# Optimization experiments

Measured on AMD Instinct MI355X. Metric: run time of the kernel, lower is better.

Reference implementation:

```python
import jax, jax.numpy as jnp
import numpy as np

B, H, W = 2, 512, 512
HID, NHKD, HEADS, KD, CD = 64, 128, 8, 16, 64
MAX_SHAPE = 512

def _conv(x, w, b=None, pad=0, groups=1):
    y = jax.lax.conv_general_dilated(x, w, (1, 1), [(pad, pad), (pad, pad)],
                                     dimension_numbers=('NCHW', 'OIHW', 'NCHW'),
                                     feature_group_count=groups)
    return y if b is None else y + b[None, :, None, None]

def _gelu(x):
    return jax.nn.gelu(x, approximate=False)  # torch nn.GELU default is exact erf

def _bn(x, s, t):
    # inference-mode BatchNorm folded to per-channel scale/shift
    return x * s[None, :, None, None] + t[None, :, None, None]

def _dyn_pos(xm, pe):
    # xm: (B, C, N); pe: (1, C, MAX_SHAPE); linear interp (align_corners=False) when N != MAX_SHAPE
    N = xm.shape[-1]
    if N != pe.shape[-1]:
        pe = jax.image.resize(pe, (1, pe.shape[1], N), method='linear')
    return xm + pe

def _sdpa(q, k, v):
    # q, k, v: (B, heads, L=key_dim, E=H); scale = 1/sqrt(E) as in F.scaled_dot_product_attention
    scale = 1.0 / np.sqrt(q.shape[-1])
    attn = jax.nn.softmax(jnp.einsum('bhie,bhje->bhij', q, k) * scale, axis=-1)
    return jnp.einsum('bhij,bhje->bhie', attn, v)

def setup_inputs():
    key = jax.random.key(0)
    ks = jax.random.split(key, 26)
    rn = lambda i, shp, sc=1.0: jax.random.normal(ks[i], shp, jnp.float32) * sc
    return {
        'x': rn(0, (B, HID, H, W)),
        'shortcut': rn(1, (B, CD, H, W)),
        'ln_w': jnp.ones((CD,), jnp.float32),
        'ln_b': jnp.zeros((CD,), jnp.float32),
        'dproj_dw_w': rn(2, (CD, 1, 3, 3), 0.2),
        'dproj_bn_s': 1.0 + rn(3, (CD,), 0.1),
        'dproj_bn_t': rn(4, (CD,), 0.1),
        'dproj_pw_w': rn(5, (2 * HID, CD, 1, 1), 0.125),
        'dproj_pw_b': rn(6, (2 * HID,), 0.05),
        'q_dw_w': rn(7, (NHKD, 1, 3, 3), 0.2),
        'q_bn_s': 1.0 + rn(8, (NHKD,), 0.1),
        'q_bn_t': rn(9, (NHKD,), 0.1),
        'k_dw_w': rn(10, (NHKD, 1, 3, 3), 0.2),
        'k_bn_s': 1.0 + rn(11, (NHKD,), 0.1),
        'k_bn_t': rn(12, (NHKD,), 0.1),
        'v_pw_w': rn(13, (NHKD, HID, 1, 1), 0.125),
        'v_bn_s': 1.0 + rn(14, (NHKD,), 0.1),
        'v_bn_t': rn(15, (NHKD,), 0.1),
        'proj_dw_w': rn(16, (HID + 2 * NHKD, 1, 3, 3), 0.2),
        'proj_dw_b': rn(17, (HID + 2 * NHKD,), 0.05),
        'proj_pw_w': rn(18, (HID, HID + 2 * NHKD, 1, 1), 0.06),
        'proj_pw_b': rn(19, (HID,), 0.05),
        'pe_rowq': rn(20, (1, NHKD, MAX_SHAPE), 0.02),
        'pe_rowk': rn(21, (1, NHKD, MAX_SHAPE), 0.02),
        'pe_colq': rn(22, (1, NHKD, MAX_SHAPE), 0.02),
        'pe_colk': rn(23, (1, NHKD, MAX_SHAPE), 0.02),
        'ape_row_w': jnp.ones((1, NHKD, 1, 1), jnp.float32),
        'ape_col_w': jnp.ones((1, NHKD, 1, 1), jnp.float32),
    }

def reference(x, shortcut, ln_w, ln_b, dproj_dw_w, dproj_bn_s, dproj_bn_t,
              dproj_pw_w, dproj_pw_b, q_dw_w, q_bn_s, q_bn_t, k_dw_w, k_bn_s,
              k_bn_t, v_pw_w, v_bn_s, v_bn_t, proj_dw_w, proj_dw_b, proj_pw_w,
              proj_pw_b, pe_rowq, pe_rowk, pe_colq, pe_colk, ape_row_w, ape_col_w):
    b, _, h, w = x.shape
    # LayerNorm2d: normalize over channel axis (biased variance, eps=1e-5)
    mu = shortcut.mean(axis=1, keepdims=True)
    var = shortcut.var(axis=1, keepdims=True)
    sn = (shortcut - mu) / jnp.sqrt(var + 1e-5) * ln_w[None, :, None, None] + ln_b[None, :, None, None]
    # d_proj: dw3x3 -> BN -> GELU -> pw1x1 -> GELU
    s = _gelu(_bn(_conv(sn, dproj_dw_w, pad=1, groups=CD), dproj_bn_s, dproj_bn_t))
    s = _gelu(_conv(s, dproj_pw_w, dproj_pw_b))
    k_in, v_in = jnp.split(s, 2, axis=1)  # each (B, HID, H, W)
    # q/k: grouped 3x3 conv (groups=HID, out=NHKD) -> BN -> GELU; v: 1x1 -> BN
    q = _gelu(_bn(_conv(x, q_dw_w, pad=1, groups=HID), q_bn_s, q_bn_t))
    k = _gelu(_bn(_conv(k_in, k_dw_w, pad=1, groups=HID), k_bn_s, k_bn_t))
    v = _bn(_conv(v_in, v_pw_w), v_bn_s, v_bn_t)
    # row attention: pool over W, seq dim = key_dim (16), head dim = H
    qr = _dyn_pos(q.mean(-1), pe_rowq).reshape(b, HEADS, KD, h)
    kr = _dyn_pos(k.mean(-1), pe_rowk).reshape(b, HEADS, KD, h)
    vr = v.mean(-1).reshape(b, HEADS, KD, h)
    attn_row = _sdpa(qr, kr, vr).reshape(b, NHKD, 1, h)
    # column attention: pool over H
    qc = _dyn_pos(q.mean(-2), pe_colq).reshape(b, HEADS, KD, w)
    kc = _dyn_pos(k.mean(-2), pe_colk).reshape(b, HEADS, KD, w)
    vc = v.mean(-2).reshape(b, HEADS, KD, w)
    attn_col = _sdpa(qc, kc, vc).reshape(b, NHKD, 1, w)
    # AxialPositionEncoding: both maps broadcast over spatial axis 2 (requires H == W)
    attn = v + ape_row_w * attn_row + ape_col_w * attn_col
    cat = jnp.concatenate([x, attn, v], axis=1)  # (B, 320, H, W)
    ctot = cat.shape[1]
    # channel shuffle: 'b (c g) h w -> b (g c) h w', g=5
    shuf = cat.reshape(b, ctot // 5, 5, h, w).transpose(0, 2, 1, 3, 4).reshape(b, ctot, h, w)
    p = _gelu(_conv(shuf, proj_dw_w, proj_dw_b, pad=1, groups=ctot))
    p = _conv(p, proj_pw_w, proj_pw_b)
    return _gelu(p)
```

## Files before the change

### kernel.cpp

```cpp
#include <hip/hip_runtime.h>
#include <math.h>

#define PLANE (512*512)

typedef short bf16x8 __attribute__((ext_vector_type(8)));
typedef float f32x4 __attribute__((ext_vector_type(4)));

__device__ __forceinline__ float gelu_f(float x) {
    float ax = fabsf(x) * 0.70710678118654752440f;
    float t = __builtin_amdgcn_rcpf(1.0f + 0.3275911f * ax);
    float poly = t * (0.254829592f + t * (-0.284496736f + t * (1.421413741f
               + t * (-1.453152027f + t * 1.061405429f))));
    float e = __expf(-ax * ax);
    float er = 1.0f - poly * e;
    er = copysignf(er, x);
    return 0.5f * x * (1.0f + er);
}

__device__ __forceinline__ unsigned short f2bf(float f) {
    union { float f; unsigned u; } v; v.f = f;
    unsigned r = v.u + 0x7FFFu + ((v.u >> 16) & 1u);
    return (unsigned short)(r >> 16);
}

__device__ __forceinline__ float bf2f(unsigned short u) {
    union { unsigned u; float f; } x; x.u = ((unsigned)u) << 16; return x.f;
}

__device__ __forceinline__ float ldval(const float* p, int off) { return p[off]; }
__device__ __forceinline__ float ldval(const unsigned short* p, int off) { return bf2f(p[off]); }

__global__ __launch_bounds__(256) void k_lnstats(const float* __restrict__ sc,
                                                 float* __restrict__ Pb,
                                                 float* __restrict__ Qb) {
    int p = blockIdx.x * 256 + threadIdx.x;
    int b = p >> 18;
    int hw = p & (PLANE - 1);
    const float* src = sc + (size_t)b * 64 * PLANE + hw;
    float sum = 0.f, sq = 0.f;
    #pragma unroll 8
    for (int c = 0; c < 64; ++c) {
        float v = src[(size_t)c * PLANE];
        sum += v; sq += v * v;
    }
    float mu = sum * (1.0f / 64.0f);
    float var = sq * (1.0f / 64.0f) - mu * mu;
    float rstd = rsqrtf(var + 1e-5f);
    Pb[p] = rstd;
    Qb[p] = -mu * rstd;
}

__global__ __launch_bounds__(256) void k_dw64ln(const float* __restrict__ sc,
                                                const float* __restrict__ dww,
                                                const float* __restrict__ lnw,
                                                const float* __restrict__ lnb,
                                                const float* __restrict__ bns,
                                                const float* __restrict__ bnt,
                                                const float* __restrict__ Pb,
                                                const float* __restrict__ Qb,
                                                unsigned* __restrict__ t1b) {
    int p = blockIdx.x * 256 + threadIdx.x;
    int b = p >> 18;
    int hw = p & (PLANE - 1);
    int h = hw >> 9, w = hw & 511;
    int tapoff[9]; float Pt[9], Qt[9], vm[9];
    const float* Pp = Pb + (size_t)b * PLANE;
    const float* Qp = Qb + (size_t)b * PLANE;
    #pragma unroll
    for (int dh = -1; dh <= 1; ++dh)
        #pragma unroll
        for (int dw = -1; dw <= 1; ++dw) {
            int k = (dh + 1) * 3 + dw + 1;
            int hh = h + dh, ww = w + dw;
            bool ok = (hh >= 0 && hh < 512 && ww >= 0 && ww < 511 + 1);
            ok = (hh >= 0 && hh < 512 && ww >= 0 && ww < 512);
            int hc = ok ? hh : h, wc = ok ? ww : w;
            int off = hc * 512 + wc;
            tapoff[k] = off;
            vm[k] = ok ? 1.f : 0.f;
            Pt[k] = Pp[off]; Qt[k] = Qp[off];
        }
    const float* scb = sc + (size_t)b * 64 * PLANE;
    unsigned* ob = t1b + (size_t)b * 32 * PLANE + hw;
    for (int c2 = 0; c2 < 32; ++c2) {
        float g[2];
        #pragma unroll
        for (int e = 0; e < 2; ++e) {
            int c = c2 * 2 + e;
            const float* wp = dww + c * 9;
            const float* cp = scb + (size_t)c * PLANE;
            float conv = 0.f, wsum = 0.f;
            #pragma unroll
            for (int k = 0; k < 9; ++k) {
                float wv = wp[k];
                float raw = cp[tapoff[k]];
                conv = fmaf(wv, fmaf(raw, Pt[k], Qt[k]) * vm[k], conv);
                wsum = fmaf(wv, vm[k], wsum);
            }
            float a = lnw[c] * conv + lnb[c] * wsum;
            g[e] = gelu_f(a * bns[c] + bnt[c]);
        }
        unsigned r;
        asm("v_cvt_pk_bf16_f32 %0,%1,%2" : "=v"(r) : "v"(g[0]), "v"(g[1]));
        ob[(size_t)c2 * PLANE] = r;
    }
}

__global__ __launch_bounds__(256) void k_wsetup2(const float* __restrict__ W1,
                                                 const float* __restrict__ W2,
                                                 unsigned short* __restrict__ w1b,
                                                 unsigned short* __restrict__ w2b) {
    int tid = blockIdx.x * 256 + threadIdx.x;
    if (tid < 8192) { w1b[tid] = f2bf(W1[tid]); w2b[tid] = f2bf(W2[tid]); }
}

__global__ __launch_bounds__(256, 4) void k_pw2(
    const unsigned* __restrict__ t1b,
    const unsigned short* __restrict__ w1b, const float* __restrict__ b1,
    const unsigned short* __restrict__ w2b,
    const float* __restrict__ vbs, const float* __restrict__ vbt,
    unsigned short* __restrict__ k_in, unsigned short* __restrict__ v)
{
    __shared__ unsigned short vin[64][88];
    __shared__ float epi[64 * 68];
    __shared__ float psl[128], ptl[128], pbl[128];
    int tid = threadIdx.x;
    if (tid < 128) { psl[tid] = vbs[tid]; ptl[tid] = vbt[tid]; pbl[tid] = b1[tid]; }
    int lane = tid & 63, wva = tid >> 6;
    int cl = lane & 15, kg = lane >> 4;
    int p0 = blockIdx.x * 64;
    int b = p0 >> 18;
    int hw0 = p0 & (PLANE - 1);
    int px = wva * 16 + cl;
    const unsigned* tp = t1b + (size_t)b * 32 * PLANE + hw0 + px;
    __syncthreads();

    unsigned bfr[2][4];
    #pragma unroll
    for (int ks = 0; ks < 2; ++ks)
        #pragma unroll
        for (int jp = 0; jp < 4; ++jp)
            bfr[ks][jp] = tp[(size_t)(ks * 16 + kg * 4 + jp) * PLANE];

    f32x4 acc[8];
    #pragma unroll
    for (int mt = 0; mt < 8; ++mt) acc[mt] = (f32x4){0.f, 0.f, 0.f, 0.f};
    #pragma unroll
    for (int ks = 0; ks < 2; ++ks) {
        union { unsigned u[4]; bf16x8 v; } bb;
        bb.u[0] = bfr[ks][0]; bb.u[1] = bfr[ks][1]; bb.u[2] = bfr[ks][2]; bb.u[3] = bfr[ks][3];
        #pragma unroll
        for (int mt = 0; mt < 8; ++mt) {
            bf16x8 af = *(const bf16x8*)(w1b + (size_t)(mt * 16 + cl) * 64 + ks * 32 + kg * 8);
            acc[mt] = __builtin_amdgcn_mfma_f32_16x16x32_bf16(af, bb.v, acc[mt], 0, 0, 0);
        }
    }

    #pragma unroll
    for (int mt = 4; mt < 8; ++mt) {
        float g[4];
        #pragma unroll
        for (int r = 0; r < 4; ++r)
            g[r] = gelu_f(acc[mt][r] + pbl[mt * 16 + kg * 4 + r]);
        unsigned r01, r23;
        asm("v_cvt_pk_bf16_f32 %0,%1,%2" : "=v"(r01) : "v"(g[0]), "v"(g[1]));
        asm("v_cvt_pk_bf16_f32 %0,%1,%2" : "=v"(r23) : "v"(g[2]), "v"(g[3]));
        int ch = (mt - 4) * 16 + kg * 4;
        *(unsigned*)&vin[px][ch]     = r01;
        *(unsigned*)&vin[px][ch + 2] = r23;
    }

    __syncthreads();
    #pragma unroll
    for (int mt = 0; mt < 4; ++mt)
        #pragma unroll
        for (int r = 0; r < 4; ++r) {
            int m = mt * 16 + kg * 4 + r;
            epi[m * 68 + px] = gelu_f(acc[mt][r] + pbl[m]);
        }
    __syncthreads();
    unsigned short* kb = k_in + (size_t)b * 64 * PLANE + hw0;
    #pragma unroll
    for (int k = 0; k < 4; ++k) {
        int m = wva * 16 + k * 4 + kg;
        float4 vv = *(const float4*)&epi[m * 68 + cl * 4];
        unsigned r01, r23;
        asm("v_cvt_pk_bf16_f32 %0,%1,%2" : "=v"(r01) : "v"(vv.x), "v"(vv.y));
        asm("v_cvt_pk_bf16_f32 %0,%1,%2" : "=v"(r23) : "v"(vv.z), "v"(vv.w));
        uint2 st; st.x = r01; st.y = r23;
        *(uint2*)&kb[(size_t)m * PLANE + cl * 4] = st;
    }

    f32x4 acc2[8];
    #pragma unroll
    for (int mt = 0; mt < 8; ++mt) acc2[mt] = (f32x4){0.f, 0.f, 0.f, 0.f};
    #pragma unroll
    for (int ks = 0; ks < 2; ++ks) {
        bf16x8 bb = *(const bf16x8*)&vin[px][ks * 32 + kg * 8];
        #pragma unroll
        for (int mt = 0; mt < 8; ++mt) {
            bf16x8 af = *(const bf16x8*)(w2b + (size_t)(mt * 16 + cl) * 64 + ks * 32 + kg * 8);
            acc2[mt] = __builtin_amdgcn_mfma_f32_16x16x32_bf16(af, bb, acc2[mt], 0, 0, 0);
        }
    }

    unsigned short* vb = v + (size_t)b * 128 * PLANE + hw0;
    #pragma unroll
    for (int pass = 0; pass < 2; ++pass) {
        __syncthreads();
        #pragma unroll
        for (int mt = pass * 4; mt < pass * 4 + 4; ++mt)
            #pragma unroll
            for (int r = 0; r < 4; ++r) {
                int m = mt * 16 + kg * 4 + r;
                epi[(m - pass * 64) * 68 + px] = acc2[mt][r] * psl[m] + ptl[m];
            }
        __syncthreads();
        #pragma unroll
        for (int k = 0; k < 4; ++k) {
            int ml = wva * 16 + k * 4 + kg;
            float4 vv = *(const float4*)&epi[ml * 68 + cl * 4];
            unsigned r01, r23;
            asm("v_cvt_pk_bf16_f32 %0,%1,%2" : "=v"(r01) : "v"(vv.x), "v"(vv.y));
            asm("v_cvt_pk_bf16_f32 %0,%1,%2" : "=v"(r23) : "v"(vv.z), "v"(vv.w));
            uint2 st; st.x = r01; st.y = r23;
            *(uint2*)&vb[(size_t)(pass * 64 + ml) * PLANE + cl * 4] = st;
        }
    }
}

template<typename T>
__global__ __launch_bounds__(512) void k_dwpool(const T* __restrict__ in,
                                                const float* __restrict__ wt,
                                                const float* __restrict__ bns,
                                                const float* __restrict__ bnt,
                                                float* __restrict__ rowsum,
                                                float* __restrict__ colpart) {
    __shared__ float lred[2][64][8];
    int tid = threadIdx.x;
    int blk = blockIdx.x;
    int hc = blk & 7;
    int g  = (blk >> 3) & 63;
    int b  = blk >> 9;
    int o0 = 2 * g, o1 = o0 + 1;
    const T* ip = in + ((size_t)b * 64 + g) * PLANE;
    float w0[9], w1[9];
    #pragma unroll
    for (int k = 0; k < 9; ++k) { w0[k] = wt[o0 * 9 + k]; w1[k] = wt[o1 * 9 + k]; }
    float s0 = bns[o0], t0 = bnt[o0], s1 = bns[o1], tt1 = bnt[o1];
    int w = tid;
    int wm = (w > 0)   ? w - 1 : w;  float vm0 = (w > 0)   ? 1.f : 0.f;
    int wp = (w < 511) ? w + 1 : w;  float vm2 = (w < 511) ? 1.f : 0.f;
    int h0 = hc * 64;
    int lane = tid & 63, wv = tid >> 6;
    float a0, a1, a2, r0, r1, r2, c0, c1, c2;
    if (h0 >= 1) {
        int o = (h0 - 1) * 512;
        a0 = ldval(ip, o + wm) * vm0; a1 = ldval(ip, o + w); a2 = ldval(ip, o + wp) * vm2;
    } else { a0 = a1 = a2 = 0.f; }
    {
        int o = h0 * 512;
        r0 = ldval(ip, o + wm) * vm0; r1 = ldval(ip, o + w); r2 = ldval(ip, o + wp) * vm2;
    }
    float ca0 = 0.f, ca1 = 0.f;
    for (int r = 0; r < 64; ++r) {
        int h = h0 + r;
        if (h + 1 <= 511) {
            int o = (h + 1) * 512;
            c0 = ldval(ip, o + wm) * vm0; c1 = ldval(ip, o + w); c2 = ldval(ip, o + wp) * vm2;
        } else { c0 = c1 = c2 = 0.f; }
        float x0 = w0[0]*a0 + w0[1]*a1 + w0[2]*a2 + w0[3]*r0 + w0[4]*r1 + w0[5]*r2
                 + w0[6]*c0 + w0[7]*c1 + w0[8]*c2;
        float x1 = w1[0]*a0 + w1[1]*a1 + w1[2]*a2 + w1[3]*r0 + w1[4]*r1 + w1[5]*r2
                 + w1[6]*c0 + w1[7]*c1 + w1[8]*c2;
        x0 = gelu_f(x0 * s0 + t0);
        x1 = gelu_f(x1 * s1 + tt1);
        ca0 += x0; ca1 += x1;
        #pragma unroll
        for (int off = 32; off > 0; off >>= 1) {
            x0 += __shfl_down(x0, off, 64);
            x1 += __shfl_down(x1, off, 64);
        }
        if (lane == 0) { lred[0][r][wv] = x0; lred[1][r][wv] = x1; }
        a0 = r0; a1 = r1; a2 = r2; r0 = c0; r1 = c1; r2 = c2;
    }
    colpart[((size_t)(b * 128 + o0) * 8 + hc) * 512 + w] = ca0;
    colpart[((size_t)(b * 128 + o1) * 8 + hc) * 512 + w] = ca1;
    __syncthreads();
    if (tid < 128) {
        int oo = tid >> 6, r = tid & 63;
        float s = 0.f;
        #pragma unroll
        for (int i = 0; i < 8; ++i) s += lred[oo][r][i];
        int och = oo ? o1 : o0;
        rowsum[((size_t)b * 128 + och) * 512 + h0 + r] = s;
    }
}

__global__ __launch_bounds__(512) void k_vpool(const unsigned short* __restrict__ v,
                                               float* __restrict__ rowsum,
                                               float* __restrict__ colpart) {
    __shared__ float lred[64][8];
    int tid = threadIdx.x;
    int blk = blockIdx.x;
    int hc = blk & 7;
    int c  = (blk >> 3) & 127;
    int b  = blk >> 10;
    int bc = b * 128 + c;
    const unsigned short* ip = v + (size_t)bc * PLANE;
    int h0 = hc * 64;
    int lane = tid & 63, wv = tid >> 6;
    float ca = 0.f;
    for (int r = 0; r < 64; ++r) {
        float a = bf2f(ip[(h0 + r) * 512 + tid]);
        ca += a;
        #pragma unroll
        for (int off = 32; off > 0; off >>= 1) a += __shfl_down(a, off, 64);
        if (lane == 0) lred[r][wv] = a;
    }
    colpart[((size_t)bc * 8 + hc) * 512 + tid] = ca;
    __syncthreads();
    if (tid < 64) {
        float s = 0.f;
        #pragma unroll
        for (int i = 0; i < 8; ++i) s += lred[tid][i];
        rowsum[(size_t)bc * 512 + h0 + tid] = s;
    }
}

__global__ __launch_bounds__(256) void k_colreduce(const float* __restrict__ part,
                                                   float* __restrict__ out, int n) {
    int idx = blockIdx.x * 256 + threadIdx.x;
    if (idx >= n) return;
    int bc = idx >> 9, w = idx & 511;
    const float* pp = part + ((size_t)bc * 8) * 512 + w;
    float s = 0.f;
    #pragma unroll
    for (int p = 0; p < 8; ++p) s += pp[p * 512];
    out[idx] = s;
}

__global__ __launch_bounds__(256) void k_attn(const float* __restrict__ qrow,
                                              const float* __restrict__ krow,
                                              const float* __restrict__ vrow,
                                              const float* __restrict__ qcol,
                                              const float* __restrict__ kcol,
                                              const float* __restrict__ vcol,
                                              const float* __restrict__ perq,
                                              const float* __restrict__ perk,
                                              const float* __restrict__ pecq,
                                              const float* __restrict__ peck,
                                              float* __restrict__ arow,
                                              float* __restrict__ acol) {
    __shared__ float P[16][17];
    int blk = blockIdx.x;
    int axis = blk & 1;
    int head = (blk >> 1) & 7;
    int b = blk >> 4;
    const float* qs = axis ? qcol : qrow;
    const float* ks = axis ? kcol : krow;
    const float* vs = axis ? vcol : vrow;
    const float* peq = axis ? pecq : perq;
    const float* pek = axis ? peck : perk;
    float* out = axis ? acol : arow;
    int tid = threadIdx.x;
    int i = tid >> 4, j = tid & 15;
    int ci = head * 16 + i, cj = head * 16 + j;
    const float* qp = qs + ((size_t)b * 128 + ci) * 512;
    const float* kp = ks + ((size_t)b * 128 + cj) * 512;
    const float* qe = peq + ci * 512;
    const float* ke = pek + cj * 512;
    float s = 0.f;
    for (int n = 0; n < 512; ++n) {
        float qv = qp[n] * (1.f / 512.f) + qe[n];
        float kv = kp[n] * (1.f / 512.f) + ke[n];
        s += qv * kv;
    }
    s *= 0.0441941738241592203f;
    P[i][j] = s;
    __syncthreads();
    if (tid < 16) {
        float mx = -1e30f;
        #pragma unroll
        for (int jj = 0; jj < 16; ++jj) mx = fmaxf(mx, P[tid][jj]);
        float e[16];
        float sum = 0.f;
        #pragma unroll
        for (int jj = 0; jj < 16; ++jj) { e[jj] = expf(P[tid][jj] - mx); sum += e[jj]; }
        float inv = 1.f / sum;
        #pragma unroll
        for (int jj = 0; jj < 16; ++jj) P[tid][jj] = e[jj] * inv;
    }
    __syncthreads();
    for (int idx = tid; idx < 16 * 512; idx += 256) {
        int ii = idx >> 9, n = idx & 511;
        const float* vb = vs + ((size_t)b * 128 + head * 16) * 512 + n;
        float acc = 0.f;
        #pragma unroll
        for (int jj = 0; jj < 16; ++jj) acc += P[ii][jj] * vb[jj * 512] * (1.f / 512.f);
        out[((size_t)b * 128 + head * 16 + ii) * 512 + n] = acc;
    }
}

__global__ __launch_bounds__(256) void k_wsetup(const float* __restrict__ pww,
                                                unsigned short* __restrict__ wsh) {
    int tid = blockIdx.x * 256 + threadIdx.x;
    if (tid >= 64 * 320) return;
    int m = tid / 320, src = tid % 320;
    int o = (src % 5) * 64 + src / 5;
    wsh[m * 320 + src] = f2bf(pww[m * 320 + o]);
}

__global__ __launch_bounds__(256) void k_awsetup(const float* __restrict__ pdw,
                                                 const float* __restrict__ aprw,
                                                 const float* __restrict__ apcw,
                                                 const float* __restrict__ arow,
                                                 const float* __restrict__ acol,
                                                 float* __restrict__ aw) {
    int idx = blockIdx.x * 256 + threadIdx.x;
    if (idx >= 2 * 128 * 512) return;
    int col = idx & 511;
    int c   = (idx >> 9) & 127;
    int b   = idx >> 16;
    int src = 64 + c;
    int o = (src % 5) * 64 + src / 5;
    const float* wd = pdw + o * 9;
    float ws0 = wd[0] + wd[3] + wd[6];
    float ws1 = wd[1] + wd[4] + wd[7];
    float ws2 = wd[2] + wd[5] + wd[8];
    const float* ar = arow + ((size_t)b * 128 + c) * 512;
    const float* ac = acol + ((size_t)b * 128 + c) * 512;
    float apr = aprw[c], apc = apcw[c];
    float sum = ws1 * (apr * ar[col] + apc * ac[col]);
    if (col > 0)   sum += ws0 * (apr * ar[col - 1] + apc * ac[col - 1]);
    if (col < 511) sum += ws2 * (apr * ar[col + 1] + apc * ac[col + 1]);
    aw[idx] = sum;
}

template<bool HE, bool WE>
__device__ __forceinline__ void conv2x2b(const unsigned short* __restrict__ p,
    const float* wlA, const float* wlP,
    const int* hrow, const float* rv, int ls, int rs, float cv0, float cv2,
    float outA[2], float outP[2])
{
    float a0,a1,a2, b0,b1,b2, c0,c1,c2;
    const unsigned short* q = p + hrow[0]*512;
    if (WE) { a0=bf2f(q[ls])*cv0; a1=bf2f(q[0]); a2=bf2f(q[rs])*cv2; } else { a0=bf2f(q[-1]); a1=bf2f(q[0]); a2=bf2f(q[1]); }
    q = p + hrow[1]*512;
    if (WE) { b0=bf2f(q[ls])*cv0; b1=bf2f(q[0]); b2=bf2f(q[rs])*cv2; } else { b0=bf2f(q[-1]); b1=bf2f(q[0]); b2=bf2f(q[1]); }
    q = p + hrow[2]*512;
    if (WE) { c0=bf2f(q[ls])*cv0; c1=bf2f(q[0]); c2=bf2f(q[rs])*cv2; } else { c0=bf2f(q[-1]); c1=bf2f(q[0]); c2=bf2f(q[1]); }
    #pragma unroll
    for (int hs = 0; hs < 2; ++hs) {
        float sA0 = wlA[0]*a0 + wlA[1]*a1 + wlA[2]*a2;
        float sA1 = wlA[3]*b0 + wlA[4]*b1 + wlA[5]*b2;
        float sA2 = wlA[6]*c0 + wlA[7]*c1 + wlA[8]*c2;
        float sP0 = wlP[0]*a0 + wlP[1]*a1 + wlP[2]*a2;
        float sP1 = wlP[3]*b0 + wlP[4]*b1 + wlP[5]*b2;
        float sP2 = wlP[6]*c0 + wlP[7]*c1 + wlP[8]*c2;
        if (HE) {
            outA[hs] = rv[hs]*sA0 + sA1 + rv[hs+2]*sA2 + wlA[9];
            outP[hs] = rv[hs]*sP0 + sP1 + rv[hs+2]*sP2 + wlP[9];
        } else {
            outA[hs] = sA0 + sA1 + sA2 + wlA[9];
            outP[hs] = sP0 + sP1 + sP2 + wlP[9];
        }
        if (hs < 1) {
            a0=b0; a1=b1; a2=b2; b0=c0; b1=c1; b2=c2;
            q = p + hrow[3]*512;
            if (WE) { c0=bf2f(q[ls])*cv0; c1=bf2f(q[0]); c2=bf2f(q[rs])*cv2; } else { c0=bf2f(q[-1]); c1=bf2f(q[0]); c2=bf2f(q[1]); }
        }
    }
}

template<bool HE, bool WE>
__device__ __forceinline__ void conv1x2(const float* __restrict__ p,
    const float* wl,
    const int* hrow, const float* rv, int ls, int rs, float cv0, float cv2,
    float out[2])
{
    float a0,a1,a2, b0,b1,b2, c0,c1,c2;
    const float* q = p + hrow[0]*512;
    if (WE) { a0=q[ls]*cv0; a1=q[0]; a2=q[rs]*cv2; } else { a0=q[-1]; a1=q[0]; a2=q[1]; }
    q = p + hrow[1]*512;
    if (WE) { b0=q[ls]*cv0; b1=q[0]; b2=q[rs]*cv2; } else { b0=q[-1]; b1=q[0]; b2=q[1]; }
    q = p + hrow[2]*512;
    if (WE) { c0=q[ls]*cv0; c1=q[0]; c2=q[rs]*cv2; } else { c0=q[-1]; c1=q[0]; c2=q[1]; }
    #pragma unroll
    for (int hs = 0; hs < 2; ++hs) {
        float s0 = wl[0]*a0 + wl[1]*a1 + wl[2]*a2;
        float s1 = wl[3]*b0 + wl[4]*b1 + wl[5]*b2;
        float s2 = wl[6]*c0 + wl[7]*c1 + wl[8]*c2;
        out[hs] = (HE ? (rv[hs]*s0 + s1 + rv[hs+2]*s2) : (s0 + s1 + s2)) + wl[9];
        if (hs < 1) {
            a0=b0; a1=b1; a2=b2; b0=c0; b1=c1; b2=c2;
            q = p + hrow[3]*512;
            if (WE) { c0=q[ls]*cv0; c1=q[0]; c2=q[rs]*cv2; } else { c0=q[-1]; c1=q[0]; c2=q[1]; }
        }
    }
}

template<bool HE, bool WE>
__device__ __forceinline__ void proj5_core(
    int h0, int wwbase, float* epi, const float* dwl,
    const float* __restrict__ xb, const unsigned short* __restrict__ vbp,
    const float* __restrict__ arb, const float* __restrict__ acb,
    const float* __restrict__ aprw, const float* __restrict__ apcw,
    const float* __restrict__ awb,
    const unsigned short* __restrict__ wsh, const float* __restrict__ pwb,
    float* __restrict__ outb)
{
    int tid = threadIdx.x;
    int lane = tid & 63, wva = tid >> 6;
    int cl = lane & 15, kg = lane >> 4;
    int ww = wwbase + wva * 16 + cl;

    int hrow[4]; float rv[4];
    #pragma unroll
    for (int i = 0; i < 4; ++i) {
        int r = h0 - 1 + i;
        float va = 1.f;
        if (HE) { if (r < 0) { r = 0; va = 0.f; } if (r > 511) { r = 511; va = 0.f; } }
        hrow[i] = r; rv[i] = va;
    }
    int ls = -1, rs = 1; float cv0 = 1.f, cv2 = 1.f;
    if (WE) {
        if (ww == 0)   { ls = 1;  cv0 = 0.f; }
        if (ww == 511) { rs = -1; cv2 = 0.f; }
    }

    f32x4 acc[2][4];
    #pragma unroll
    for (int hs = 0; hs < 2; ++hs)
        #pragma unroll
        for (int mt = 0; mt < 4; ++mt)
            acc[hs][mt] = (f32x4){0.f, 0.f, 0.f, 0.f};

    #pragma unroll
    for (int ks = 0; ks < 2; ++ks) {
        unsigned bp[2][4];
        #pragma unroll
        for (int jp = 0; jp < 4; ++jp) {
            float cj0[2], cj1[2];
            int ch = ks * 32 + kg * 8 + jp * 2;
            conv1x2<HE,WE>(xb + (size_t)ch * PLANE + ww, dwl + ch * 12,
                           hrow, rv, ls, rs, cv0, cv2, cj0);
            conv1x2<HE,WE>(xb + (size_t)(ch+1) * PLANE + ww, dwl + (ch+1) * 12,
                           hrow, rv, ls, rs, cv0, cv2, cj1);
            #pragma unroll
            for (int hs = 0; hs < 2; ++hs) {
                float g0 = gelu_f(cj0[hs]), g1 = gelu_f(cj1[hs]);
                unsigned r;
                asm("v_cvt_pk_bf16_f32 %0,%1,%2" : "=v"(r) : "v"(g0), "v"(g1));
                bp[hs][jp] = r;
            }
        }
        #pragma unroll
        for (int mt = 0; mt < 4; ++mt) {
            bf16x8 af = *(const bf16x8*)(wsh + (size_t)(mt * 16 + cl) * 320 + ks * 32 + kg * 8);
            #pragma unroll
            for (int hs = 0; hs < 2; ++hs) {
                union { unsigned u[4]; bf16x8 v; } bb;
                bb.u[0] = bp[hs][0]; bb.u[1] = bp[hs][1]; bb.u[2] = bp[hs][2]; bb.u[3] = bp[hs][3];
                acc[hs][mt] = __builtin_amdgcn_mfma_f32_16x16x32_bf16(af, bb.v, acc[hs][mt], 0, 0, 0);
            }
        }
    }

    #pragma unroll
    for (int vks = 0; vks < 4; ++vks) {
        unsigned bpA[2][4], bpP[2][4];
        #pragma unroll
        for (int jp = 0; jp < 4; ++jp) {
            float cA[2][2], cP[2][2];
            #pragma unroll
            for (int e = 0; e < 2; ++e) {
                int c = vks * 32 + kg * 8 + jp * 2 + e;
                const float* wlA = dwl + (64 + c) * 12;
                conv2x2b<HE,WE>(vbp + (size_t)c * PLANE + ww, wlA, dwl + (192 + c) * 12,
                                hrow, rv, ls, rs, cv0, cv2, cA[e], cP[e]);
                float awv = awb[(size_t)c * 512 + ww];
                #pragma unroll
                for (int hs = 0; hs < 2; ++hs) {
                    if (!HE) {
                        cA[e][hs] += awv;
                    } else {
                        if (rv[hs] + rv[hs + 2] == 2.f) {
                            cA[e][hs] += awv;
                        } else {
                            const float* arp = arb + (size_t)c * 512 + ww;
                            const float* acp = acb + (size_t)c * 512 + ww;
                            float apr = aprw[c], apc = apcw[c];
                            float aa0 = (apr * arp[ls] + apc * acp[ls]) * cv0;
                            float aa1 =  apr * arp[0]  + apc * acp[0];
                            float aa2 = (apr * arp[rs] + apc * acp[rs]) * cv2;
                            float wd0 = rv[hs]*wlA[0] + wlA[3] + rv[hs+2]*wlA[6];
                            float wd1 = rv[hs]*wlA[1] + wlA[4] + rv[hs+2]*wlA[7];
                            float wd2 = rv[hs]*wlA[2] + wlA[5] + rv[hs+2]*wlA[8];
                            cA[e][hs] += wd0*aa0 + wd1*aa1 + wd2*aa2;
                        }
                    }
                }
            }
            #pragma unroll
            for (int hs = 0; hs < 2; ++hs) {
                float gA0 = gelu_f(cA[0][hs]), gA1 = gelu_f(cA[1][hs]);
                float gP0 = gelu_f(cP[0][hs]), gP1 = gelu_f(cP[1][hs]);
                unsigned ra, rp;
                asm("v_cvt_pk_bf16_f32 %0,%1,%2" : "=v"(ra) : "v"(gA0), "v"(gA1));
                asm("v_cvt_pk_bf16_f32 %0,%1,%2" : "=v"(rp) : "v"(gP0), "v"(gP1));
                bpA[hs][jp] = ra; bpP[hs][jp] = rp;
            }
        }
        #pragma unroll
        for (int mt = 0; mt < 4; ++mt) {
            bf16x8 afA = *(const bf16x8*)(wsh + (size_t)(mt * 16 + cl) * 320 + (2 + vks) * 32 + kg * 8);
            #pragma unroll
            for (int hs = 0; hs < 2; ++hs) {
                union { unsigned u[4]; bf16x8 v; } bb;
                bb.u[0] = bpA[hs][0]; bb.u[1] = bpA[hs][1]; bb.u[2] = bpA[hs][2]; bb.u[3] = bpA[hs][3];
                acc[hs][mt] = __builtin_amdgcn_mfma_f32_16x16x32_bf16(afA, bb.v, acc[hs][mt], 0, 0, 0);
            }
            bf16x8 afP = *(const bf16x8*)(wsh + (size_t)(mt * 16 + cl) * 320 + (6 + vks) * 32 + kg * 8);
            #pragma unroll
            for (int hs = 0; hs < 2; ++hs) {
                union { unsigned u[4]; bf16x8 v; } bb;
                bb.u[0] = bpP[hs][0]; bb.u[1] = bpP[hs][1]; bb.u[2] = bpP[hs][2]; bb.u[3] = bpP[hs][3];
                acc[hs][mt] = __builtin_amdgcn_mfma_f32_16x16x32_bf16(afP, bb.v, acc[hs][mt], 0, 0, 0);
            }
        }
    }

    #pragma unroll
    for (int hs = 0; hs < 2; ++hs) {
        __syncthreads();
        #pragma unroll
        for (int mt = 0; mt < 4; ++mt)
            #pragma unroll
            for (int r = 0; r < 4; ++r) {
                int m = mt * 16 + kg * 4 + r;
                epi[m * 68 + wva * 16 + cl] = gelu_f(acc[hs][mt][r] + pwb[m]);
            }
        __syncthreads();
        #pragma unroll
        for (int k = 0; k < 4; ++k) {
            int m = wva * 16 + k * 4 + kg;
            float4 vv = *(const float4*)&epi[m * 68 + cl * 4];
            *(float4*)&outb[(size_t)m * PLANE + (size_t)(h0 + hs) * 512 + wwbase + cl * 4] = vv;
        }
    }
}

__global__ __launch_bounds__(256, 4) void k_proj5(
    const float* __restrict__ x, const unsigned short* __restrict__ v,
    const float* __restrict__ arow, const float* __restrict__ acol,
    const float* __restrict__ aprw, const float* __restrict__ apcw,
    const float* __restrict__ dww, const float* __restrict__ dwb,
    const unsigned short* __restrict__ wsh, const float* __restrict__ pwb,
    const float* __restrict__ aw, float* __restrict__ out)
{
    __shared__ float dwl[320 * 12];
    __shared__ float epi[64 * 68];
    int tid = threadIdx.x;
    for (int i = tid; i < 3200; i += 256) {
        int src = i / 10, k = i - src * 10;
        int o = (src % 5) * 64 + src / 5;
        dwl[src * 12 + k] = (k < 9) ? dww[o * 9 + k] : dwb[o];
    }
    __syncthreads();
    int flat = blockIdx.x;
    int nf = (flat & 7) * 512 + (flat >> 3);
    int bx = nf & 7;
    int s  = (nf >> 3) & 255;
    int b  = nf >> 11;
    int h0 = s * 2, wwbase = bx * 64;
    const float* xb  = x + (size_t)b * 64 * PLANE;
    const unsigned short* vbp = v + (size_t)b * 128 * PLANE;
    const float* arb = arow + (size_t)b * 128 * 512;
    const float* acb = acol + (size_t)b * 128 * 512;
    const float* awb = aw + (size_t)b * 128 * 512;
    float* outb = out + (size_t)b * 64 * PLANE;
    bool HEr = (s == 0) || (s == 255);
    bool WEr = (bx == 0) || (bx == 7);
    if (!HEr && !WEr)
        proj5_core<false,false>(h0, wwbase, epi, dwl, xb, vbp, arb, acb, aprw, apcw, awb, wsh, pwb, outb);
    else if (!HEr)
        proj5_core<false,true >(h0, wwbase, epi, dwl, xb, vbp, arb, acb, aprw, apcw, awb, wsh, pwb, outb);
    else
        proj5_core<true ,true >(h0, wwbase, epi, dwl, xb, vbp, arb, acb, aprw, apcw, awb, wsh, pwb, outb);
}

extern "C" void kernel_launch(void* const* d_in, const int* in_sizes, int n_in,
                              void* d_out, int out_size, void* d_ws, size_t ws_size,
                              hipStream_t stream) {
    const float* x    = (const float*)d_in[0];
    const float* sc   = (const float*)d_in[1];
    const float* lnw  = (const float*)d_in[2];
    const float* lnb  = (const float*)d_in[3];
    const float* ddw  = (const float*)d_in[4];
    const float* dbs  = (const float*)d_in[5];
    const float* dbt  = (const float*)d_in[6];
    const float* pw1  = (const float*)d_in[7];
    const float* pb1  = (const float*)d_in[8];
    const float* qdw  = (const float*)d_in[9];
    const float* qbs  = (const float*)d_in[10];
    const float* qbt  = (const float*)d_in[11];
    const float* kdw  = (const float*)d_in[12];
    const float* kbs  = (const float*)d_in[13];
    const float* kbt  = (const float*)d_in[14];
    const float* vpw  = (const float*)d_in[15];
    const float* vbs  = (const float*)d_in[16];
    const float* vbt  = (const float*)d_in[17];
    const float* pdw  = (const float*)d_in[18];
    const float* pdb  = (const float*)d_in[19];
    const float* ppw  = (const float*)d_in[20];
    const float* ppb  = (const float*)d_in[21];
    const float* perq = (const float*)d_in[22];
    const float* perk = (const float*)d_in[23];
    const float* pecq = (const float*)d_in[24];
    const float* peck = (const float*)d_in[25];
    const float* aprw = (const float*)d_in[26];
    const float* apcw = (const float*)d_in[27];

    unsigned short* kin_b = (unsigned short*)d_out;
    float* ws   = (float*)d_ws;
    float* bufB = ws;
    unsigned short* v_b = (unsigned short*)(ws + 33554432);
    float* sm   = ws + 100663296;
    float* qrow = sm;
    float* krow = sm + 131072;
    float* vrow = sm + 262144;
    float* qcol = sm + 393216;
    float* kcol = sm + 524288;
    float* vcol = sm + 655360;
    float* arow = sm + 786432;
    float* acol = sm + 917504;
    unsigned short* wsh = (unsigned short*)(ws + 101711872);
    float* aw   = ws + 101722112;
    unsigned short* w1b = (unsigned short*)(ws + 101853184);
    unsigned short* w2b = (unsigned short*)(ws + 101857280);
    float* Pb   = ws + 101861376;
    float* Qb   = ws + 102385664;
    unsigned* t1b = (unsigned*)bufB;
    float* qcp  = bufB;
    float* kcp  = bufB + 1048576;
    float* vcp  = bufB + 2097152;

    k_wsetup <<<80,   256, 0, stream>>>(ppw, wsh);
    k_wsetup2<<<32,   256, 0, stream>>>(pw1, vpw, w1b, w2b);
    k_lnstats<<<2048, 256, 0, stream>>>(sc, Pb, Qb);
    k_dw64ln <<<2048, 256, 0, stream>>>(sc, ddw, lnw, lnb, dbs, dbt, Pb, Qb, t1b);
    k_pw2    <<<8192, 256, 0, stream>>>(t1b, w1b, pb1, w2b, vbs, vbt, kin_b, v_b);
    k_dwpool<unsigned short><<<1024, 512, 0, stream>>>(kin_b, kdw, kbs, kbt, krow, kcp);
    k_vpool  <<<2048, 512, 0, stream>>>(v_b, vrow, vcp);
    k_dwpool<float><<<1024, 512, 0, stream>>>(x, qdw, qbs, qbt, qrow, qcp);
    k_colreduce<<<1536, 256, 0, stream>>>(qcp, qcol, 393216);
    k_attn   <<<32,   256, 0, stream>>>(qrow, krow, vrow, qcol, kcol, vcol,
                                        perq, perk, pecq, peck, arow, acol);
    k_awsetup<<<512,  256, 0, stream>>>(pdw, aprw, apcw, arow, acol, aw);
    k_proj5  <<<4096, 256, 0, stream>>>(x, v_b, arow, acol, aprw, apcw,
                                        pdw, pdb, wsh, ppb, aw, (float*)d_out);
}
```

Measured before the change: 912.6 us.

## Parallelize axial attention across query rows and use tanh-form GELU

The attention kernel now launches one block per (batch, axis, head, query row) and splits each QK dot product across 16 lanes with a shuffle reduction, replacing 32 blocks of long serial loops. Softmax normalization is folded into the output scaling. GELU switches from the erf polynomial to a cheaper sigmoid-based tanh approximation, which changes numerics relative to exact erf GELU. The new attention recomputes the per-head V pass redundantly per query row.

```diff
diff --git a/kernel.cpp b/kernel.cpp
--- a/kernel.cpp
+++ b/kernel.cpp
@@ -7,14 +7,10 @@
 typedef float f32x4 __attribute__((ext_vector_type(4)));
 
 __device__ __forceinline__ float gelu_f(float x) {
-    float ax = fabsf(x) * 0.70710678118654752440f;
-    float t = __builtin_amdgcn_rcpf(1.0f + 0.3275911f * ax);
-    float poly = t * (0.254829592f + t * (-0.284496736f + t * (1.421413741f
-               + t * (-1.453152027f + t * 1.061405429f))));
-    float e = __expf(-ax * ax);
-    float er = 1.0f - poly * e;
-    er = copysignf(er, x);
-    return 0.5f * x * (1.0f + er);
+    float t2 = fmaf(x * x, 0.0713548162f, 1.5957691216f);
+    float e = __expf(x * t2);
+    float r = __builtin_amdgcn_rcpf(1.0f + e);
+    return fmaf(-x, r, x);
 }
 
 __device__ __forceinline__ unsigned short f2bf(float f) {
@@ -72,8 +68,7 @@
         for (int dw = -1; dw <= 1; ++dw) {
             int k = (dh + 1) * 3 + dw + 1;
             int hh = h + dh, ww = w + dw;
-            bool ok = (hh >= 0 && hh < 512 && ww >= 0 && ww < 511 + 1);
-            ok = (hh >= 0 && hh < 512 && ww >= 0 && ww < 512);
+            bool ok = (hh >= 0 && hh < 512 && ww >= 0 && ww < 512);
             int hc = ok ? hh : h, wc = ok ? ww : w;
             int off = hc * 512 + wc;
             tapoff[k] = off;
@@ -352,11 +347,13 @@
                                               const float* __restrict__ peck,
                                               float* __restrict__ arow,
                                               float* __restrict__ acol) {
-    __shared__ float P[16][17];
+    __shared__ float Pj[16];
+    __shared__ float Pe[16];
     int blk = blockIdx.x;
-    int axis = blk & 1;
-    int head = (blk >> 1) & 7;
-    int b = blk >> 4;
+    int i    = blk & 15;
+    int head = (blk >> 4) & 7;
+    int axis = (blk >> 7) & 1;
+    int b    = blk >> 8;
     const float* qs = axis ? qcol : qrow;
     const float* ks = axis ? kcol : krow;
     const float* vs = axis ? vcol : vrow;
@@ -364,41 +361,44 @@
     const float* pek = axis ? peck : perk;
     float* out = axis ? acol : arow;
     int tid = threadIdx.x;
-    int i = tid >> 4, j = tid & 15;
+    int j = tid >> 4, l = tid & 15;
     int ci = head * 16 + i, cj = head * 16 + j;
     const float* qp = qs + ((size_t)b * 128 + ci) * 512;
     const float* kp = ks + ((size_t)b * 128 + cj) * 512;
     const float* qe = peq + ci * 512;
     const float* ke = pek + cj * 512;
     float s = 0.f;
-    for (int n = 0; n < 512; ++n) {
+    int n0 = l * 32;
+    for (int n = n0; n < n0 + 32; ++n) {
         float qv = qp[n] * (1.f / 512.f) + qe[n];
         float kv = kp[n] * (1.f / 512.f) + ke[n];
-        s += qv * kv;
-    }
-    s *= 0.0441941738241592203f;
-    P[i][j] = s;
+        s = fmaf(qv, kv, s);
+    }
+    #pragma unroll
+    for (int off = 8; off > 0; off >>= 1) s += __shfl_down(s, off, 16);
+    if (l == 0) Pj[j] = s * 0.0441941738241592203f;
     __syncthreads();
     if (tid < 16) {
         float mx = -1e30f;
         #pragma unroll
-        for (int jj = 0; jj < 16; ++jj) mx = fmaxf(mx, P[tid][jj]);
-        float e[16];
-        float sum = 0.f;
-        #pragma unroll
-        for (int jj = 0; jj < 16; ++jj) { e[jj] = expf(P[tid][jj] - mx); sum += e[jj]; }
-        float inv = 1.f / sum;
-        #pragma unroll
-        for (int jj = 0; jj < 16; ++jj) P[tid][jj] = e[jj] * inv;
+        for (int jj = 0; jj < 16; ++jj) mx = fmaxf(mx, Pj[jj]);
+        Pe[tid] = expf(Pj[tid] - mx);
     }
     __syncthreads();
-    for (int idx = tid; idx < 16 * 512; idx += 256) {
-        int ii = idx >> 9, n = idx & 511;
-        const float* vb = vs + ((size_t)b * 128 + head * 16) * 512 + n;
+    float sum = 0.f;
+    #pragma unroll
+    for (int jj = 0; jj < 16; ++jj) sum += Pe[jj];
+    float inv = (1.f / 512.f) / sum;
+    const float* vb = vs + ((size_t)b * 128 + head * 16) * 512;
+    float* op = out + ((size_t)b * 128 + ci) * 512;
+    #pragma unroll
+    for (int rep = 0; rep < 2; ++rep) {
+        int n = rep * 256 + tid;
         float acc = 0.f;
         #pragma unroll
-        for (int jj = 0; jj < 16; ++jj) acc += P[ii][jj] * vb[jj * 512] * (1.f / 512.f);
-        out[((size_t)b * 128 + head * 16 + ii) * 512 + n] = acc;
+        for (int jj = 0; jj < 16; ++jj)
+            acc = fmaf(Pe[jj], vb[jj * 512 + n], acc);
+        op[n] = acc * inv;
     }
 }
 
@@ -755,7 +755,7 @@
     k_vpool  <<<2048, 512, 0, stream>>>(v_b, vrow, vcp);
     k_dwpool<float><<<1024, 512, 0, stream>>>(x, qdw, qbs, qbt, qrow, qcp);
     k_colreduce<<<1536, 256, 0, stream>>>(qcp, qcol, 393216);
-    k_attn   <<<32,   256, 0, stream>>>(qrow, krow, vrow, qcol, kcol, vcol,
+    k_attn   <<<512,  256, 0, stream>>>(qrow, krow, vrow, qcol, kcol, vcol,
                                         perq, perk, pecq, peck, arow, acol);
     k_awsetup<<<512,  256, 0, stream>>>(pdw, aprw, apcw, arow, acol, aw);
     k_proj5  <<<4096, 256, 0, stream>>>(x, v_b, arow, acol, aprw, apcw,
```

Result: faster. 856.3 us, median of 2 (-6.2%).
